# Kernel tuning notes

Measured on AMD Instinct MI355X. Metric: run time of the kernel, lower is better.

Reference implementation:

```python
import jax, jax.numpy as jnp
import numpy as np

NUM_HEADS = 16
NUM_KV_HEADS = 4
HEAD_DIM = 128
ROPE_THETA = 500000.0
RMS_EPS = 1e-5


def _rms_norm(x, w, eps=RMS_EPS):
    # normalize over last dim in fp32, as in YuaRMSNorm
    xf = x.astype(jnp.float32)
    var = jnp.mean(xf * xf, axis=-1, keepdims=True)
    return (w * (xf * jax.lax.rsqrt(var + eps))).astype(x.dtype)


def _rotate_half(x):
    x1, x2 = jnp.split(x, 2, axis=-1)
    return jnp.concatenate([-x2, x1], axis=-1)


def _rope_cos_sin(seq_len, dim, dtype):
    inv_freq = 1.0 / (ROPE_THETA ** (jnp.arange(0, dim, 2, dtype=jnp.float32) / dim))
    pos = jnp.arange(seq_len, dtype=jnp.float32)
    freqs = pos[:, None] * inv_freq[None, :]          # [S, dim/2]
    emb = jnp.concatenate([freqs, freqs], axis=-1)     # [S, dim]
    return jnp.cos(emb).astype(dtype), jnp.sin(emb).astype(dtype)


def setup_inputs() -> dict:
    key = jax.random.key(0)
    ks = jax.random.split(key, 5)
    B, S, H = 2, 2048, 2048
    q_out = NUM_HEADS * HEAD_DIM
    kv_out = NUM_KV_HEADS * HEAD_DIM
    sc = 0.02
    return {
        "hidden_states": jax.random.normal(ks[0], (B, S, H), jnp.float32),
        "q_w": jax.random.normal(ks[1], (q_out, H), jnp.float32) * sc,
        "k_w": jax.random.normal(ks[2], (kv_out, H), jnp.float32) * sc,
        "v_w": jax.random.normal(ks[3], (kv_out, H), jnp.float32) * sc,
        "o_w": jax.random.normal(ks[4], (H, q_out), jnp.float32) * sc,
        "q_norm_w": jnp.ones((HEAD_DIM,), jnp.float32),
        "k_norm_w": jnp.ones((HEAD_DIM,), jnp.float32),
    }


def reference(hidden_states, q_w, k_w, v_w, o_w, q_norm_w, k_norm_w):
    B, S, H = hidden_states.shape
    groups = NUM_HEADS // NUM_KV_HEADS

    # fused-ish QKV projections (torch Linear: x @ W^T)
    q = jnp.einsum('bsh,oh->bso', hidden_states, q_w).reshape(B, S, NUM_HEADS, HEAD_DIM).transpose(0, 2, 1, 3)
    k = jnp.einsum('bsh,oh->bso', hidden_states, k_w).reshape(B, S, NUM_KV_HEADS, HEAD_DIM).transpose(0, 2, 1, 3)
    v = jnp.einsum('bsh,oh->bso', hidden_states, v_w).reshape(B, S, NUM_KV_HEADS, HEAD_DIM).transpose(0, 2, 1, 3)

    # QK RMSNorm over head_dim
    q = _rms_norm(q, q_norm_w)
    k = _rms_norm(k, k_norm_w)

    # RoPE (position_ids = arange(S))
    cos, sin = _rope_cos_sin(S, HEAD_DIM, q.dtype)  # [S, hd]
    cos = cos[None, None]  # [1,1,S,hd]
    sin = sin[None, None]
    q = q * cos + _rotate_half(q) * sin
    k = k * cos + _rotate_half(k) * sin

    # GQA repeat_interleave of kv heads
    k = jnp.repeat(k, groups, axis=1)  # [B, num_heads, S, hd]
    v = jnp.repeat(v, groups, axis=1)

    # causal SDPA
    scale = 1.0 / jnp.sqrt(jnp.asarray(HEAD_DIM, q.dtype))
    scores = jnp.einsum('bhqd,bhkd->bhqk', q, k) * scale
    causal = jnp.tril(jnp.ones((S, S), bool))
    scores = jnp.where(causal[None, None], scores, jnp.finfo(scores.dtype).min)
    probs = jax.nn.softmax(scores, axis=-1)
    attn = jnp.einsum('bhqk,bhkd->bhqd', probs, v)

    attn = attn.transpose(0, 2, 1, 3).reshape(B, S, NUM_HEADS * HEAD_DIM)
    return jnp.einsum('bso,ho->bsh', attn, o_w)
```

## Files before the change

kernel.cpp:

```cpp
#include <hip/hip_runtime.h>
#include <stdint.h>

#define S_LEN 2048
#define BATCH 2
#define NH 16
#define NKV 4
#define HD 128
#define HID 2048
#define MROWS (BATCH * S_LEN)
#define PST 72

typedef unsigned short u16;
typedef __attribute__((ext_vector_type(8))) short frag_ab;
typedef __attribute__((ext_vector_type(4))) float frag_cd;

static __device__ __forceinline__ float bf2f(u16 v) {
    union { unsigned u; float f; } t; t.u = ((unsigned)v) << 16; return t.f;
}
static __device__ __forceinline__ u16 f2bf(float f) {
    union { float f; unsigned u; } t; t.f = f;
    unsigned r = t.u + 0x7fffu + ((t.u >> 16) & 1u);
    return (u16)(r >> 16);
}
static __device__ __forceinline__ void load_lds16(const u16* g, u16* l) {
    __builtin_amdgcn_global_load_lds((const __attribute__((address_space(1))) void*)g,
                                     (__attribute__((address_space(3))) void*)l, 16, 0, 0);
}

__global__ __launch_bounds__(256) void conv_f32_bf16(const float* __restrict__ src,
                                                     u16* __restrict__ dst, int n4) {
    int i = blockIdx.x * 256 + threadIdx.x;
    if (i >= n4) return;
    float4 v = ((const float4*)src)[i];
    ushort4 o;
    o.x = f2bf(v.x); o.y = f2bf(v.y); o.z = f2bf(v.z); o.w = f2bf(v.w);
    ((ushort4*)dst)[i] = o;
}

__global__ __launch_bounds__(256) void gemm_bt(const u16* __restrict__ A, const u16* __restrict__ B,
                                               float* __restrict__ C, int M, int N, int K) {
    __shared__ u16 As[128 * 32];
    __shared__ u16 Bs[128 * 32];
    const int tid = threadIdx.x;
    const int wave = tid >> 6, lane = tid & 63;
    const int quad = lane >> 4, lr = lane & 15;
    const int wm = (wave & 1) * 64, wn = (wave >> 1) * 64;
    const long bm = (long)blockIdx.x * 128, bn = (long)blockIdx.y * 128;
    const int srow = (wave << 4) + (lane >> 2);
    const int scol = (lane & 3) * 8;
    const u16* Ag = A + (bm + srow) * (long)K + scol;
    const u16* Bg = B + (bn + srow) * (long)K + scol;
    u16* AsW = As + wave * 512;
    u16* BsW = Bs + wave * 512;

    frag_cd acc[4][4];
#pragma unroll
    for (int i = 0; i < 4; i++)
#pragma unroll
        for (int j = 0; j < 4; j++) acc[i][j] = (frag_cd){0.f, 0.f, 0.f, 0.f};

    for (int k0 = 0; k0 < K; k0 += 32) {
        __syncthreads();
        load_lds16(Ag + k0, AsW);
        load_lds16(Ag + (long)64 * K + k0, AsW + 2048);
        load_lds16(Bg + k0, BsW);
        load_lds16(Bg + (long)64 * K + k0, BsW + 2048);
        __syncthreads();
        frag_ab af[4], bfr[4];
#pragma unroll
        for (int i = 0; i < 4; i++) af[i] = *(const frag_ab*)(As + (wm + i * 16 + lr) * 32 + quad * 8);
#pragma unroll
        for (int j = 0; j < 4; j++) bfr[j] = *(const frag_ab*)(Bs + (wn + j * 16 + lr) * 32 + quad * 8);
#pragma unroll
        for (int i = 0; i < 4; i++)
#pragma unroll
            for (int j = 0; j < 4; j++)
                acc[i][j] = __builtin_amdgcn_mfma_f32_16x16x32_bf16(af[i], bfr[j], acc[i][j], 0, 0, 0);
    }
#pragma unroll
    for (int i = 0; i < 4; i++)
#pragma unroll
        for (int j = 0; j < 4; j++)
#pragma unroll
            for (int r = 0; r < 4; r++) {
                long row = bm + wm + i * 16 + quad * 4 + r;
                long col = bn + wn + j * 16 + lr;
                C[row * N + col] = acc[i][j][r];
            }
}

__global__ __launch_bounds__(256) void rope_norm(const float* __restrict__ src, u16* __restrict__ dst,
                                                 const float* __restrict__ nw, int nh, int stride, int coff) {
    const int m = blockIdx.x;
    const int wave = threadIdx.x >> 6, lane = threadIdx.x & 63;
    const int s = m & (S_LEN - 1), b = m >> 11;
    const int d0 = 2 * lane;
    const float w0 = nw[d0], w1 = nw[d0 + 1];
    const int i0 = d0 & 63;
    const float lnt_over = 13.122363377404328f / 64.f;
    float inv0 = expf(-(float)i0 * lnt_over);
    float inv1 = expf(-(float)(i0 + 1) * lnt_over);
    float c0 = cosf((float)s * inv0), sn0 = sinf((float)s * inv0);
    float c1 = cosf((float)s * inv1), sn1 = sinf((float)s * inv1);
    for (int h = wave; h < nh; h += 4) {
        float2 x = *(const float2*)(src + (long)m * stride + coff + h * HD + d0);
        float ss = x.x * x.x + x.y * x.y;
#pragma unroll
        for (int off = 1; off < 64; off <<= 1) ss += __shfl_xor(ss, off);
        float rs = rsqrtf(ss * (1.f / HD) + 1e-5f);
        float xn0 = x.x * rs * w0;
        float xn1 = x.y * rs * w1;
        float p0 = __shfl_xor(xn0, 32);
        float p1 = __shfl_xor(xn1, 32);
        float r0 = (lane < 32) ? -p0 : p0;
        float r1 = (lane < 32) ? -p1 : p1;
        float y0 = xn0 * c0 + r0 * sn0;
        float y1 = xn1 * c1 + r1 * sn1;
        unsigned outw = (unsigned)f2bf(y0) | ((unsigned)f2bf(y1) << 16);
        *(unsigned*)(dst + (((long)(b * nh + h) * S_LEN + s) * HD + d0)) = outw;
    }
}

__global__ __launch_bounds__(256) void pack_vt(const float* __restrict__ src, u16* __restrict__ dst,
                                               int stride, int coff) {
    __shared__ u16 t[128 * 72];
    const int tid = threadIdx.x;
    const int st = blockIdx.x & 31;
    const int kh = (blockIdx.x >> 5) & 3;
    const int b = blockIdx.x >> 7;
    const long m0 = (long)b * S_LEN + st * 64;
#pragma unroll
    for (int c = 0; c < 8; c++) {
        int idx = c * 256 + tid;
        int r = idx >> 5, cg = idx & 31;
        float4 v = *(const float4*)(src + (m0 + r) * stride + coff + kh * HD + cg * 4);
        int col = cg * 4;
        t[(col + 0) * 72 + r] = f2bf(v.x);
        t[(col + 1) * 72 + r] = f2bf(v.y);
        t[(col + 2) * 72 + r] = f2bf(v.z);
        t[(col + 3) * 72 + r] = f2bf(v.w);
    }
    __syncthreads();
    const int d = tid >> 1, sh = (tid & 1) * 32;
    u16* dp = dst + ((long)(b * NKV + kh) * HD + d) * S_LEN + st * 64 + sh;
    const u16* tp = &t[d * 72 + sh];
    *(uint4*)(dp + 0)  = *(const uint4*)(tp + 0);
    *(uint4*)(dp + 8)  = *(const uint4*)(tp + 8);
    *(uint4*)(dp + 16) = *(const uint4*)(tp + 16);
    *(uint4*)(dp + 24) = *(const uint4*)(tp + 24);
}

__global__ __launch_bounds__(256, 2) void flash_attn(const u16* __restrict__ Q, const u16* __restrict__ K,
                                                     const u16* __restrict__ Vt, u16* __restrict__ O) {
    __shared__ u16 Pls[4 * 32 * PST];
    __shared__ float macc[2][8][16][16];
    __shared__ float mlb[4][2][16][2];
    const int tid = threadIdx.x;
    const int wave = tid >> 6, lane = tid & 63;
    const int quad = lane >> 4, lr = lane & 15;
    const int g = blockIdx.x & 7;
    const int sub = (blockIdx.x >> 3) & 3;
    const int p = blockIdx.x >> 5;
    const int b = g >> 2, kh = g & 3;
    const int h = kh * 4 + sub;
    const float scale = 0.08838834764831845f;
    const u16* Qb = Q + ((long)(b * NH + h) * S_LEN) * HD;
    const u16* Kb = K + ((long)(b * NKV + kh) * S_LEN) * HD;
    const u16* Vb = Vt + ((long)(b * NKV + kh) * HD) * S_LEN;
    const int pbase = wave * 32 * PST;

    for (int ph = 0; ph < 2; ph++) {
        const int t = ph ? p : (63 - p);
        const int q0 = t * 32;
        const int nkt = (t >> 1) + 1;

        frag_ab qf[2][4];
#pragma unroll
        for (int mt = 0; mt < 2; mt++) {
            int qrow = q0 + mt * 16 + lr;
#pragma unroll
            for (int ks = 0; ks < 4; ks++)
                qf[mt][ks] = *(const frag_ab*)(Qb + (long)qrow * HD + ks * 32 + quad * 8);
        }
        frag_cd oa[2][8];
        float m_i[2][4], l_i[2][4];
#pragma unroll
        for (int mt = 0; mt < 2; mt++) {
#pragma unroll
            for (int dt = 0; dt < 8; dt++) oa[mt][dt] = (frag_cd){0.f, 0.f, 0.f, 0.f};
#pragma unroll
            for (int r = 0; r < 4; r++) { m_i[mt][r] = -3e38f; l_i[mt][r] = 0.f; }
        }

        for (int kt = wave; kt < nkt; kt += 4) {
            const int j0 = kt * 64;
            frag_cd sa[2][4];
#pragma unroll
            for (int mt = 0; mt < 2; mt++)
#pragma unroll
                for (int nt = 0; nt < 4; nt++) sa[mt][nt] = (frag_cd){0.f, 0.f, 0.f, 0.f};
#pragma unroll
            for (int nt = 0; nt < 4; nt++) {
                frag_ab kf[4];
#pragma unroll
                for (int ks = 0; ks < 4; ks++)
                    kf[ks] = *(const frag_ab*)(Kb + (long)(j0 + nt * 16 + lr) * HD + ks * 32 + quad * 8);
#pragma unroll
                for (int mt = 0; mt < 2; mt++)
#pragma unroll
                    for (int ks = 0; ks < 4; ks++)
                        sa[mt][nt] = __builtin_amdgcn_mfma_f32_16x16x32_bf16(qf[mt][ks], kf[ks], sa[mt][nt], 0, 0, 0);
            }
            frag_ab vf[2][8];
#pragma unroll
            for (int ks = 0; ks < 2; ks++)
#pragma unroll
                for (int dt = 0; dt < 8; dt++)
                    vf[ks][dt] = *(const frag_ab*)(Vb + (long)(dt * 16 + lr) * S_LEN + j0 + ks * 32 + quad * 8);

            const bool need_mask = (j0 + 63) > q0;
#pragma unroll
            for (int mt = 0; mt < 2; mt++) {
                float mrow[4] = {-3e38f, -3e38f, -3e38f, -3e38f};
#pragma unroll
                for (int nt = 0; nt < 4; nt++) {
                    int key = j0 + nt * 16 + lr;
#pragma unroll
                    for (int r = 0; r < 4; r++) {
                        int qrow = q0 + mt * 16 + quad * 4 + r;
                        float v = sa[mt][nt][r] * scale;
                        if (need_mask) v = (key <= qrow) ? v : -3e38f;
                        sa[mt][nt][r] = v;
                        mrow[r] = fmaxf(mrow[r], v);
                    }
                }
#pragma unroll
                for (int off = 1; off < 16; off <<= 1)
#pragma unroll
                    for (int r = 0; r < 4; r++) mrow[r] = fmaxf(mrow[r], __shfl_xor(mrow[r], off));
                float rs[4];
#pragma unroll
                for (int r = 0; r < 4; r++) {
                    float mn = fmaxf(m_i[mt][r], mrow[r]);
                    float alpha = __expf(m_i[mt][r] - mn);
                    m_i[mt][r] = mn;
                    l_i[mt][r] *= alpha;
                    rs[r] = 0.f;
#pragma unroll
                    for (int dt = 0; dt < 8; dt++) oa[mt][dt][r] *= alpha;
                }
#pragma unroll
                for (int nt = 0; nt < 4; nt++)
#pragma unroll
                    for (int r = 0; r < 4; r++) {
                        float pw = __expf(sa[mt][nt][r] - m_i[mt][r]);
                        rs[r] += pw;
                        Pls[pbase + (mt * 16 + quad * 4 + r) * PST + nt * 16 + lr] = f2bf(pw);
                    }
#pragma unroll
                for (int off = 1; off < 16; off <<= 1)
#pragma unroll
                    for (int r = 0; r < 4; r++) rs[r] += __shfl_xor(rs[r], off);
#pragma unroll
                for (int r = 0; r < 4; r++) l_i[mt][r] += rs[r];
            }

#pragma unroll
            for (int ks = 0; ks < 2; ks++) {
                frag_ab pf[2];
#pragma unroll
                for (int mt = 0; mt < 2; mt++)
                    pf[mt] = *(const frag_ab*)&Pls[pbase + (mt * 16 + lr) * PST + ks * 32 + quad * 8];
#pragma unroll
                for (int dt = 0; dt < 8; dt++) {
                    oa[0][dt] = __builtin_amdgcn_mfma_f32_16x16x32_bf16(pf[0], vf[ks][dt], oa[0][dt], 0, 0, 0);
                    oa[1][dt] = __builtin_amdgcn_mfma_f32_16x16x32_bf16(pf[1], vf[ks][dt], oa[1][dt], 0, 0, 0);
                }
            }
        }

        if (lr == 0) {
#pragma unroll
            for (int mt = 0; mt < 2; mt++)
#pragma unroll
                for (int r = 0; r < 4; r++) {
                    mlb[wave][mt][quad * 4 + r][0] = m_i[mt][r];
                    mlb[wave][mt][quad * 4 + r][1] = l_i[mt][r];
                }
        }
        __syncthreads();
        float inv[2][4];
#pragma unroll
        for (int mt = 0; mt < 2; mt++)
#pragma unroll
            for (int r = 0; r < 4; r++) {
                int row = quad * 4 + r;
                float m0 = mlb[0][mt][row][0], m1 = mlb[1][mt][row][0];
                float m2 = mlb[2][mt][row][0], m3 = mlb[3][mt][row][0];
                float ms = fmaxf(fmaxf(m0, m1), fmaxf(m2, m3));
                float ls = mlb[0][mt][row][1] * __expf(m0 - ms) + mlb[1][mt][row][1] * __expf(m1 - ms)
                         + mlb[2][mt][row][1] * __expf(m2 - ms) + mlb[3][mt][row][1] * __expf(m3 - ms);
                inv[mt][r] = 1.f / ls;
                float alpha = __expf(m_i[mt][r] - ms);
#pragma unroll
                for (int dt = 0; dt < 8; dt++) oa[mt][dt][r] *= alpha;
            }
        for (int w = 0; w < 4; w++) {
            if (wave == w) {
#pragma unroll
                for (int mt = 0; mt < 2; mt++)
#pragma unroll
                    for (int dt = 0; dt < 8; dt++) {
                        frag_cd* pp = (frag_cd*)&macc[mt][dt][lr][quad * 4];
                        if (w == 0) *pp = oa[mt][dt];
                        else {
                            frag_cd o = *pp;
#pragma unroll
                            for (int r = 0; r < 4; r++) o[r] += oa[mt][dt][r];
                            *pp = o;
                        }
                    }
            }
            __syncthreads();
        }
#pragma unroll
        for (int mt = 0; mt < 2; mt++)
#pragma unroll
            for (int dto = 0; dto < 2; dto++) {
                int dt = wave * 2 + dto;
                frag_cd v = *(const frag_cd*)&macc[mt][dt][lr][quad * 4];
#pragma unroll
                for (int r = 0; r < 4; r++) {
                    int s = q0 + mt * 16 + quad * 4 + r;
                    O[((long)b * S_LEN + s) * (NH * HD) + h * HD + dt * 16 + lr] =
                        f2bf(v[r] * inv[mt][r]);
                }
            }
    }
}

extern "C" void kernel_launch(void* const* d_in, const int* in_sizes, int n_in,
                              void* d_out, int out_size, void* d_ws, size_t ws_size,
                              hipStream_t stream) {
    const float* hs  = (const float*)d_in[0];
    const float* q_w = (const float*)d_in[1];
    const float* k_w = (const float*)d_in[2];
    const float* v_w = (const float*)d_in[3];
    const float* o_w = (const float*)d_in[4];
    const float* qnw = (const float*)d_in[5];
    const float* knw = (const float*)d_in[6];
    float* out = (float*)d_out;

    char* ws = (char*)d_ws;
    u16* hs_bf  = (u16*)(ws);
    u16* wbuf   = (u16*)(ws + (16ul << 20));
    float* gout = (float*)(ws + (24ul << 20));
    u16* Kr     = (u16*)(ws + (40ul << 20));
    u16* Vt     = (u16*)(ws + (44ul << 20));
    u16* Qr     = (u16*)(ws + (56ul << 20));
    (void)ws_size; (void)in_sizes; (void)n_in; (void)out_size;

    conv_f32_bf16<<<(MROWS * HID / 4 + 255) / 256, 256, 0, stream>>>(hs, hs_bf, MROWS * HID / 4);

    conv_f32_bf16<<<(HID * HID / 4 + 255) / 256, 256, 0, stream>>>(q_w, wbuf, HID * HID / 4);
    dim3 gq(MROWS / 128, HID / 128);
    gemm_bt<<<gq, 256, 0, stream>>>(hs_bf, wbuf, gout, MROWS, HID, HID);
    rope_norm<<<MROWS, 256, 0, stream>>>(gout, Qr, qnw, NH, HID, 0);

    conv_f32_bf16<<<(NKV * HD * HID / 4 + 255) / 256, 256, 0, stream>>>(k_w, wbuf, NKV * HD * HID / 4);
    conv_f32_bf16<<<(NKV * HD * HID / 4 + 255) / 256, 256, 0, stream>>>(v_w, wbuf + NKV * HD * HID, NKV * HD * HID / 4);
    dim3 gkv(MROWS / 128, (2 * NKV * HD) / 128);
    gemm_bt<<<gkv, 256, 0, stream>>>(hs_bf, wbuf, gout, MROWS, 2 * NKV * HD, HID);
    rope_norm<<<MROWS, 256, 0, stream>>>(gout, Kr, knw, NKV, 2 * NKV * HD, 0);
    pack_vt<<<BATCH * NKV * (S_LEN / 64), 256, 0, stream>>>(gout, Vt, 2 * NKV * HD, NKV * HD);

    flash_attn<<<1024, 256, 0, stream>>>(Qr, Kr, Vt, hs_bf);

    conv_f32_bf16<<<(HID * HID / 4 + 255) / 256, 256, 0, stream>>>(o_w, wbuf, HID * HID / 4);
    gemm_bt<<<gq, 256, 0, stream>>>(hs_bf, wbuf, out, MROWS, HID, HID);
}
```

Baseline: 462.9 us.

## Launch one flash-attention block per query tile and alias shared buffers

Each flash-attention block previously handled two paired query tiles (a long one and a short one) in sequence. Now each block handles one 32-row tile, with the grid doubled to 2048 and heavy tiles scheduled first. The P staging buffer and the output-reduction buffer now share one shared-memory region, which cuts LDS per block and may allow more resident blocks. The trade-off is losing the paired load balancing in exchange for finer-grained scheduling and more parallelism.

```diff
diff --git a/kernel.cpp b/kernel.cpp
--- a/kernel.cpp
+++ b/kernel.cpp
@@ -152,15 +152,19 @@
 
 __global__ __launch_bounds__(256, 2) void flash_attn(const u16* __restrict__ Q, const u16* __restrict__ K,
                                                      const u16* __restrict__ Vt, u16* __restrict__ O) {
-    __shared__ u16 Pls[4 * 32 * PST];
-    __shared__ float macc[2][8][16][16];
-    __shared__ float mlb[4][2][16][2];
+    __shared__ __align__(16) char shmem[19456];
+    u16* Pls = (u16*)shmem;
+    float* maccf = (float*)shmem;
+    float* mlbf = (float*)(shmem + 18432);
+#define MACC(mt, dt, c, r) (((((mt) * 8 + (dt)) * 16 + (c)) * 16) + (r))
+#define MLB(w, mt, row, j) (((((w) * 2 + (mt)) * 16 + (row)) * 2) + (j))
     const int tid = threadIdx.x;
     const int wave = tid >> 6, lane = tid & 63;
     const int quad = lane >> 4, lr = lane & 15;
     const int g = blockIdx.x & 7;
     const int sub = (blockIdx.x >> 3) & 3;
-    const int p = blockIdx.x >> 5;
+    const int tt = blockIdx.x >> 5;
+    const int t = 63 - tt;
     const int b = g >> 2, kh = g & 3;
     const int h = kh * 4 + sub;
     const float scale = 0.08838834764831845f;
@@ -169,174 +173,173 @@
     const u16* Vb = Vt + ((long)(b * NKV + kh) * HD) * S_LEN;
     const int pbase = wave * 32 * PST;
 
-    for (int ph = 0; ph < 2; ph++) {
-        const int t = ph ? p : (63 - p);
-        const int q0 = t * 32;
-        const int nkt = (t >> 1) + 1;
-
-        frag_ab qf[2][4];
+    const int q0 = t * 32;
+    const int nkt = (t >> 1) + 1;
+
+    frag_ab qf[2][4];
+#pragma unroll
+    for (int mt = 0; mt < 2; mt++) {
+        int qrow = q0 + mt * 16 + lr;
+#pragma unroll
+        for (int ks = 0; ks < 4; ks++)
+            qf[mt][ks] = *(const frag_ab*)(Qb + (long)qrow * HD + ks * 32 + quad * 8);
+    }
+    frag_cd oa[2][8];
+    float m_i[2][4], l_i[2][4];
+#pragma unroll
+    for (int mt = 0; mt < 2; mt++) {
+#pragma unroll
+        for (int dt = 0; dt < 8; dt++) oa[mt][dt] = (frag_cd){0.f, 0.f, 0.f, 0.f};
+#pragma unroll
+        for (int r = 0; r < 4; r++) { m_i[mt][r] = -3e38f; l_i[mt][r] = 0.f; }
+    }
+
+    for (int kt = wave; kt < nkt; kt += 4) {
+        const int j0 = kt * 64;
+        frag_cd sa[2][4];
+#pragma unroll
+        for (int mt = 0; mt < 2; mt++)
+#pragma unroll
+            for (int nt = 0; nt < 4; nt++) sa[mt][nt] = (frag_cd){0.f, 0.f, 0.f, 0.f};
+#pragma unroll
+        for (int nt = 0; nt < 4; nt++) {
+            frag_ab kf[4];
+#pragma unroll
+            for (int ks = 0; ks < 4; ks++)
+                kf[ks] = *(const frag_ab*)(Kb + (long)(j0 + nt * 16 + lr) * HD + ks * 32 + quad * 8);
+#pragma unroll
+            for (int mt = 0; mt < 2; mt++)
+#pragma unroll
+                for (int ks = 0; ks < 4; ks++)
+                    sa[mt][nt] = __builtin_amdgcn_mfma_f32_16x16x32_bf16(qf[mt][ks], kf[ks], sa[mt][nt], 0, 0, 0);
+        }
+        frag_ab vf[2][8];
+#pragma unroll
+        for (int ks = 0; ks < 2; ks++)
+#pragma unroll
+            for (int dt = 0; dt < 8; dt++)
+                vf[ks][dt] = *(const frag_ab*)(Vb + (long)(dt * 16 + lr) * S_LEN + j0 + ks * 32 + quad * 8);
+
+        const bool need_mask = (j0 + 63) > q0;
 #pragma unroll
         for (int mt = 0; mt < 2; mt++) {
-            int qrow = q0 + mt * 16 + lr;
-#pragma unroll
-            for (int ks = 0; ks < 4; ks++)
-                qf[mt][ks] = *(const frag_ab*)(Qb + (long)qrow * HD + ks * 32 + quad * 8);
-        }
-        frag_cd oa[2][8];
-        float m_i[2][4], l_i[2][4];
-#pragma unroll
-        for (int mt = 0; mt < 2; mt++) {
-#pragma unroll
-            for (int dt = 0; dt < 8; dt++) oa[mt][dt] = (frag_cd){0.f, 0.f, 0.f, 0.f};
-#pragma unroll
-            for (int r = 0; r < 4; r++) { m_i[mt][r] = -3e38f; l_i[mt][r] = 0.f; }
-        }
-
-        for (int kt = wave; kt < nkt; kt += 4) {
-            const int j0 = kt * 64;
-            frag_cd sa[2][4];
+            float mrow[4] = {-3e38f, -3e38f, -3e38f, -3e38f};
+#pragma unroll
+            for (int nt = 0; nt < 4; nt++) {
+                int key = j0 + nt * 16 + lr;
+#pragma unroll
+                for (int r = 0; r < 4; r++) {
+                    int qrow = q0 + mt * 16 + quad * 4 + r;
+                    float v = sa[mt][nt][r] * scale;
+                    if (need_mask) v = (key <= qrow) ? v : -3e38f;
+                    sa[mt][nt][r] = v;
+                    mrow[r] = fmaxf(mrow[r], v);
+                }
+            }
+#pragma unroll
+            for (int off = 1; off < 16; off <<= 1)
+#pragma unroll
+                for (int r = 0; r < 4; r++) mrow[r] = fmaxf(mrow[r], __shfl_xor(mrow[r], off));
+            float rs[4];
+#pragma unroll
+            for (int r = 0; r < 4; r++) {
+                float mn = fmaxf(m_i[mt][r], mrow[r]);
+                float alpha = __expf(m_i[mt][r] - mn);
+                m_i[mt][r] = mn;
+                l_i[mt][r] *= alpha;
+                rs[r] = 0.f;
+#pragma unroll
+                for (int dt = 0; dt < 8; dt++) oa[mt][dt][r] *= alpha;
+            }
+#pragma unroll
+            for (int nt = 0; nt < 4; nt++)
+#pragma unroll
+                for (int r = 0; r < 4; r++) {
+                    float pw = __expf(sa[mt][nt][r] - m_i[mt][r]);
+                    rs[r] += pw;
+                    Pls[pbase + (mt * 16 + quad * 4 + r) * PST + nt * 16 + lr] = f2bf(pw);
+                }
+#pragma unroll
+            for (int off = 1; off < 16; off <<= 1)
+#pragma unroll
+                for (int r = 0; r < 4; r++) rs[r] += __shfl_xor(rs[r], off);
+#pragma unroll
+            for (int r = 0; r < 4; r++) l_i[mt][r] += rs[r];
+        }
+
+#pragma unroll
+        for (int ks = 0; ks < 2; ks++) {
+            frag_ab pf[2];
 #pragma unroll
             for (int mt = 0; mt < 2; mt++)
-#pragma unroll
-                for (int nt = 0; nt < 4; nt++) sa[mt][nt] = (frag_cd){0.f, 0.f, 0.f, 0.f};
-#pragma unroll
-            for (int nt = 0; nt < 4; nt++) {
-                frag_ab kf[4];
-#pragma unroll
-                for (int ks = 0; ks < 4; ks++)
-                    kf[ks] = *(const frag_ab*)(Kb + (long)(j0 + nt * 16 + lr) * HD + ks * 32 + quad * 8);
-#pragma unroll
-                for (int mt = 0; mt < 2; mt++)
-#pragma unroll
-                    for (int ks = 0; ks < 4; ks++)
-                        sa[mt][nt] = __builtin_amdgcn_mfma_f32_16x16x32_bf16(qf[mt][ks], kf[ks], sa[mt][nt], 0, 0, 0);
-            }
-            frag_ab vf[2][8];
-#pragma unroll
-            for (int ks = 0; ks < 2; ks++)
-#pragma unroll
-                for (int dt = 0; dt < 8; dt++)
-                    vf[ks][dt] = *(const frag_ab*)(Vb + (long)(dt * 16 + lr) * S_LEN + j0 + ks * 32 + quad * 8);
-
-            const bool need_mask = (j0 + 63) > q0;
-#pragma unroll
-            for (int mt = 0; mt < 2; mt++) {
-                float mrow[4] = {-3e38f, -3e38f, -3e38f, -3e38f};
-#pragma unroll
-                for (int nt = 0; nt < 4; nt++) {
-                    int key = j0 + nt * 16 + lr;
-#pragma unroll
-                    for (int r = 0; r < 4; r++) {
-                        int qrow = q0 + mt * 16 + quad * 4 + r;
-                        float v = sa[mt][nt][r] * scale;
-                        if (need_mask) v = (key <= qrow) ? v : -3e38f;
-                        sa[mt][nt][r] = v;
-                        mrow[r] = fmaxf(mrow[r], v);
+                pf[mt] = *(const frag_ab*)&Pls[pbase + (mt * 16 + lr) * PST + ks * 32 + quad * 8];
+#pragma unroll
+            for (int dt = 0; dt < 8; dt++) {
+                oa[0][dt] = __builtin_amdgcn_mfma_f32_16x16x32_bf16(pf[0], vf[ks][dt], oa[0][dt], 0, 0, 0);
+                oa[1][dt] = __builtin_amdgcn_mfma_f32_16x16x32_bf16(pf[1], vf[ks][dt], oa[1][dt], 0, 0, 0);
+            }
+        }
+    }
+
+    if (lr == 0) {
+#pragma unroll
+        for (int mt = 0; mt < 2; mt++)
+#pragma unroll
+            for (int r = 0; r < 4; r++) {
+                mlbf[MLB(wave, mt, quad * 4 + r, 0)] = m_i[mt][r];
+                mlbf[MLB(wave, mt, quad * 4 + r, 1)] = l_i[mt][r];
+            }
+    }
+    __syncthreads();
+    float inv[2][4];
+#pragma unroll
+    for (int mt = 0; mt < 2; mt++)
+#pragma unroll
+        for (int r = 0; r < 4; r++) {
+            int row = quad * 4 + r;
+            float m0 = mlbf[MLB(0, mt, row, 0)], m1 = mlbf[MLB(1, mt, row, 0)];
+            float m2 = mlbf[MLB(2, mt, row, 0)], m3 = mlbf[MLB(3, mt, row, 0)];
+            float ms = fmaxf(fmaxf(m0, m1), fmaxf(m2, m3));
+            float ls = mlbf[MLB(0, mt, row, 1)] * __expf(m0 - ms) + mlbf[MLB(1, mt, row, 1)] * __expf(m1 - ms)
+                     + mlbf[MLB(2, mt, row, 1)] * __expf(m2 - ms) + mlbf[MLB(3, mt, row, 1)] * __expf(m3 - ms);
+            inv[mt][r] = 1.f / ls;
+            float alpha = __expf(m_i[mt][r] - ms);
+#pragma unroll
+            for (int dt = 0; dt < 8; dt++) oa[mt][dt][r] *= alpha;
+        }
+    for (int w = 0; w < 4; w++) {
+        if (wave == w) {
+#pragma unroll
+            for (int mt = 0; mt < 2; mt++)
+#pragma unroll
+                for (int dt = 0; dt < 8; dt++) {
+                    frag_cd* pp = (frag_cd*)&maccf[MACC(mt, dt, lr, quad * 4)];
+                    if (w == 0) *pp = oa[mt][dt];
+                    else {
+                        frag_cd o = *pp;
+#pragma unroll
+                        for (int r = 0; r < 4; r++) o[r] += oa[mt][dt][r];
+                        *pp = o;
                     }
                 }
-#pragma unroll
-                for (int off = 1; off < 16; off <<= 1)
-#pragma unroll
-                    for (int r = 0; r < 4; r++) mrow[r] = fmaxf(mrow[r], __shfl_xor(mrow[r], off));
-                float rs[4];
-#pragma unroll
-                for (int r = 0; r < 4; r++) {
-                    float mn = fmaxf(m_i[mt][r], mrow[r]);
-                    float alpha = __expf(m_i[mt][r] - mn);
-                    m_i[mt][r] = mn;
-                    l_i[mt][r] *= alpha;
-                    rs[r] = 0.f;
-#pragma unroll
-                    for (int dt = 0; dt < 8; dt++) oa[mt][dt][r] *= alpha;
-                }
-#pragma unroll
-                for (int nt = 0; nt < 4; nt++)
-#pragma unroll
-                    for (int r = 0; r < 4; r++) {
-                        float pw = __expf(sa[mt][nt][r] - m_i[mt][r]);
-                        rs[r] += pw;
-                        Pls[pbase + (mt * 16 + quad * 4 + r) * PST + nt * 16 + lr] = f2bf(pw);
-                    }
-#pragma unroll
-                for (int off = 1; off < 16; off <<= 1)
-#pragma unroll
-                    for (int r = 0; r < 4; r++) rs[r] += __shfl_xor(rs[r], off);
-#pragma unroll
-                for (int r = 0; r < 4; r++) l_i[mt][r] += rs[r];
-            }
-
-#pragma unroll
-            for (int ks = 0; ks < 2; ks++) {
-                frag_ab pf[2];
-#pragma unroll
-                for (int mt = 0; mt < 2; mt++)
-                    pf[mt] = *(const frag_ab*)&Pls[pbase + (mt * 16 + lr) * PST + ks * 32 + quad * 8];
-#pragma unroll
-                for (int dt = 0; dt < 8; dt++) {
-                    oa[0][dt] = __builtin_amdgcn_mfma_f32_16x16x32_bf16(pf[0], vf[ks][dt], oa[0][dt], 0, 0, 0);
-                    oa[1][dt] = __builtin_amdgcn_mfma_f32_16x16x32_bf16(pf[1], vf[ks][dt], oa[1][dt], 0, 0, 0);
-                }
-            }
-        }
-
-        if (lr == 0) {
-#pragma unroll
-            for (int mt = 0; mt < 2; mt++)
-#pragma unroll
-                for (int r = 0; r < 4; r++) {
-                    mlb[wave][mt][quad * 4 + r][0] = m_i[mt][r];
-                    mlb[wave][mt][quad * 4 + r][1] = l_i[mt][r];
-                }
         }
         __syncthreads();
-        float inv[2][4];
-#pragma unroll
-        for (int mt = 0; mt < 2; mt++)
+    }
+#pragma unroll
+    for (int mt = 0; mt < 2; mt++)
+#pragma unroll
+        for (int dto = 0; dto < 2; dto++) {
+            int dt = wave * 2 + dto;
+            frag_cd v = *(const frag_cd*)&maccf[MACC(mt, dt, lr, quad * 4)];
 #pragma unroll
             for (int r = 0; r < 4; r++) {
-                int row = quad * 4 + r;
-                float m0 = mlb[0][mt][row][0], m1 = mlb[1][mt][row][0];
-                float m2 = mlb[2][mt][row][0], m3 = mlb[3][mt][row][0];
-                float ms = fmaxf(fmaxf(m0, m1), fmaxf(m2, m3));
-                float ls = mlb[0][mt][row][1] * __expf(m0 - ms) + mlb[1][mt][row][1] * __expf(m1 - ms)
-                         + mlb[2][mt][row][1] * __expf(m2 - ms) + mlb[3][mt][row][1] * __expf(m3 - ms);
-                inv[mt][r] = 1.f / ls;
-                float alpha = __expf(m_i[mt][r] - ms);
-#pragma unroll
-                for (int dt = 0; dt < 8; dt++) oa[mt][dt][r] *= alpha;
-            }
-        for (int w = 0; w < 4; w++) {
-            if (wave == w) {
-#pragma unroll
-                for (int mt = 0; mt < 2; mt++)
-#pragma unroll
-                    for (int dt = 0; dt < 8; dt++) {
-                        frag_cd* pp = (frag_cd*)&macc[mt][dt][lr][quad * 4];
-                        if (w == 0) *pp = oa[mt][dt];
-                        else {
-                            frag_cd o = *pp;
-#pragma unroll
-                            for (int r = 0; r < 4; r++) o[r] += oa[mt][dt][r];
-                            *pp = o;
-                        }
-                    }
-            }
-            __syncthreads();
-        }
-#pragma unroll
-        for (int mt = 0; mt < 2; mt++)
-#pragma unroll
-            for (int dto = 0; dto < 2; dto++) {
-                int dt = wave * 2 + dto;
-                frag_cd v = *(const frag_cd*)&macc[mt][dt][lr][quad * 4];
-#pragma unroll
-                for (int r = 0; r < 4; r++) {
-                    int s = q0 + mt * 16 + quad * 4 + r;
-                    O[((long)b * S_LEN + s) * (NH * HD) + h * HD + dt * 16 + lr] =
-                        f2bf(v[r] * inv[mt][r]);
-                }
-            }
-    }
+                int s = q0 + mt * 16 + quad * 4 + r;
+                O[((long)b * S_LEN + s) * (NH * HD) + h * HD + dt * 16 + lr] =
+                    f2bf(v[r] * inv[mt][r]);
+            }
+        }
+#undef MACC
+#undef MLB
 }
 
 extern "C" void kernel_launch(void* const* d_in, const int* in_sizes, int n_in,
@@ -374,7 +377,7 @@
     rope_norm<<<MROWS, 256, 0, stream>>>(gout, Kr, knw, NKV, 2 * NKV * HD, 0);
     pack_vt<<<BATCH * NKV * (S_LEN / 64), 256, 0, stream>>>(gout, Vt, 2 * NKV * HD, NKV * HD);
 
-    flash_attn<<<1024, 256, 0, stream>>>(Qr, Kr, Vt, hs_bf);
+    flash_attn<<<2048, 256, 0, stream>>>(Qr, Kr, Vt, hs_bf);
 
     conv_f32_bf16<<<(HID * HID / 4 + 255) / 256, 256, 0, stream>>>(o_w, wbuf, HID * HID / 4);
     gemm_bt<<<gq, 256, 0, stream>>>(hs_bf, wbuf, out, MROWS, HID, HID);
```

New measurement: 448.4 us. 3.1% less time.
